# Performance work log

Hardware: AMD Instinct MI355X
Metric: run time of the kernel (lower is better)

Reference implementation:

```python
import jax, jax.numpy as jnp
import numpy as np

EMBED = 256
NHEAD = 8
DFF = 1024
NLAYERS = 1
B, H, W, WS = 4, 128, 128, 16


def _layernorm(x, g, b, eps=1e-5):
    mu = jnp.mean(x, axis=-1, keepdims=True)
    var = jnp.var(x, axis=-1, keepdims=True)
    return (x - mu) * jax.lax.rsqrt(var + eps) * g + b


def _mha(q, k, v, in_w, in_b, out_w, out_b, kpm=None):
    # torch nn.MultiheadAttention (batch_first) with dropout=0
    Bn, L, C = q.shape
    dh = C // NHEAD
    wq, wk, wv = jnp.split(in_w, 3, axis=0)
    bq, bk, bv = jnp.split(in_b, 3, axis=0)
    qh = (q @ wq.T + bq).reshape(Bn, L, NHEAD, dh)
    kh = (k @ wk.T + bk).reshape(Bn, k.shape[1], NHEAD, dh)
    vh = (v @ wv.T + bv).reshape(Bn, v.shape[1], NHEAD, dh)
    scores = jnp.einsum('bqhd,bkhd->bhqk', qh, kh) * (dh ** -0.5)
    if kpm is not None:  # True == masked key
        scores = jnp.where(kpm[:, None, None, :], -jnp.inf, scores)
    attn = jax.nn.softmax(scores, axis=-1)
    out = jnp.einsum('bhqk,bkhd->bqhd', attn, vh).reshape(Bn, L, C)
    return out @ out_w.T + out_b


def _enc_layer(q, k, v, p, kpm=None):
    # post-norm AxisPermutedEncoderLayer, dropout=0
    (in_w, in_b, out_w, out_b, l1w, l1b, l2w, l2b, g1, b1, g2, b2) = p
    src = v + _mha(q, k, v, in_w, in_b, out_w, out_b, kpm)
    src = _layernorm(src, g1, b1)
    ff = jax.nn.relu(src @ l1w.T + l1b) @ l2w.T + l2b
    return _layernorm(src + ff, g2, b2)


def _forward(backbone_memory, defe_feature_filtered, window_size, glob_pos_embed,
             rel_w1, rel_b1, rel_w2, rel_b2,
             in_proj_w, in_proj_b, out_proj_w, out_proj_b,
             lin1_w, lin1_b, lin2_w, lin2_b, ln1_g, ln1_b, ln2_g, ln2_b):
    Bb, C, Hh, Ww = backbone_memory.shape
    ws = window_size
    nwh, nww = Hh // ws, Ww // ws
    nw, T = nwh * nww, ws * ws
    p = (in_proj_w, in_proj_b, out_proj_w, out_proj_b,
         lin1_w, lin1_b, lin2_w, lin2_b, ln1_g, ln1_b, ln2_g, ln2_b)
    # relative position embedding: MLP over normalized in-window (y,x) coords
    ys, xs = jnp.meshgrid(jnp.arange(ws), jnp.arange(ws), indexing='ij')
    coords = jnp.stack([ys, xs], -1).reshape(T, 2).astype(backbone_memory.dtype) / max(ws - 1, 1)
    rel = jax.nn.relu(coords @ rel_w1.T + rel_b1) @ rel_w2.T + rel_b2  # [T,C]
    # window partition -> [B, nw, T, C]
    feats = backbone_memory.reshape(Bb, C, nwh, ws, nww, ws).transpose(0, 2, 4, 1, 3, 5)
    feats = feats.reshape(Bb, nw, C, T).transpose(0, 1, 3, 2)
    gp = glob_pos_embed.reshape(C, nwh, ws, nww, ws).transpose(1, 3, 0, 2, 4)
    gp = gp.reshape(nw, C, T).transpose(0, 2, 1)[None]  # [1,nw,T,C]
    pos = jnp.broadcast_to(gp + rel[None, None], (Bb, nw, T, C))
    # window validity via max-pool of binary map
    pooled = defe_feature_filtered.reshape(Bb, 1, nwh, ws, nww, ws).max(axis=(3, 5))
    valid = pooled.reshape(Bb, nw) > 0  # bool [B,nw]
    x = feats
    for _ in range(NLAYERS):
        # within-window attention over T tokens
        wi = x.reshape(Bb * nw, T, C)
        wp = pos.reshape(Bb * nw, T, C)
        x = _enc_layer(wi + wp, wi + wp, wi, p).reshape(Bb, nw, T, C)
        # cross-window attention over nw windows (per token position)
        ci = x.transpose(0, 2, 1, 3).reshape(Bb * T, nw, C)
        cp = pos.transpose(0, 2, 1, 3).reshape(Bb * T, nw, C)
        kpm = jnp.broadcast_to(~valid[:, None, :], (Bb, T, nw)).reshape(Bb * T, nw)
        x = _enc_layer(ci + cp, ci + cp, ci, p, kpm).reshape(Bb, T, nw, C).transpose(0, 2, 1, 3)
    enc = x.transpose(0, 1, 3, 2).reshape(Bb, nw, C, ws, ws)
    enc = enc * valid.astype(x.dtype)[:, :, None, None, None]
    upd = enc.reshape(Bb, nwh, nww, C, ws, ws).transpose(0, 3, 1, 4, 2, 5).reshape(Bb, C, Hh, Ww)
    return backbone_memory + upd, valid


def setup_inputs() -> dict:
    key = jax.random.key(0)
    ks = jax.random.split(key, 16)
    C, s = EMBED, 0.02
    inp = {}
    inp['backbone_memory'] = jax.random.normal(ks[0], (B, C, H, W), jnp.float32)
    inp['defe_feature_filtered'] = (jax.random.uniform(ks[1], (B, 1, H, W)) < 0.002).astype(jnp.float32)
    inp['window_size'] = WS
    inp['glob_pos_embed'] = jax.random.normal(ks[2], (C, H, W), jnp.float32) * s
    inp['rel_w1'] = jax.random.normal(ks[3], (64, 2), jnp.float32) * s
    inp['rel_b1'] = jnp.zeros((64,), jnp.float32)
    inp['rel_w2'] = jax.random.normal(ks[4], (C, 64), jnp.float32) * s
    inp['rel_b2'] = jnp.zeros((C,), jnp.float32)
    inp['in_proj_w'] = jax.random.normal(ks[5], (3 * C, C), jnp.float32) * s
    inp['in_proj_b'] = jnp.zeros((3 * C,), jnp.float32)
    inp['out_proj_w'] = jax.random.normal(ks[6], (C, C), jnp.float32) * s
    inp['out_proj_b'] = jnp.zeros((C,), jnp.float32)
    inp['lin1_w'] = jax.random.normal(ks[7], (DFF, C), jnp.float32) * s
    inp['lin1_b'] = jnp.zeros((DFF,), jnp.float32)
    inp['lin2_w'] = jax.random.normal(ks[8], (C, DFF), jnp.float32) * s
    inp['lin2_b'] = jnp.zeros((C,), jnp.float32)
    inp['ln1_g'] = jnp.ones((C,), jnp.float32)
    inp['ln1_b'] = jnp.zeros((C,), jnp.float32)
    inp['ln2_g'] = jnp.ones((C,), jnp.float32)
    inp['ln2_b'] = jnp.zeros((C,), jnp.float32)
    return inp


def reference(backbone_memory, defe_feature_filtered, window_size, glob_pos_embed,
              rel_w1, rel_b1, rel_w2, rel_b2,
              in_proj_w, in_proj_b, out_proj_w, out_proj_b,
              lin1_w, lin1_b, lin2_w, lin2_b, ln1_g, ln1_b, ln2_g, ln2_b):
    return _forward(backbone_memory, defe_feature_filtered, window_size, glob_pos_embed,
                    rel_w1, rel_b1, rel_w2, rel_b2,
                    in_proj_w, in_proj_b, out_proj_w, out_proj_b,
                    lin1_w, lin1_b, lin2_w, lin2_b, ln1_g, ln1_b, ln2_g, ln2_b)
```

## Files before the change

### kernel.cpp

```cpp
#include <hip/hip_runtime.h>
#include <hip/hip_bf16.h>

#define CEMB 256
#define NHEAD 8
#define DHEAD 32
#define DFF 1024
#define BB 4
#define HH 128
#define WW 128
#define WSZ 16
#define NWH 8
#define NW 64
#define TT 256
#define NTOK (BB*NW*TT)

typedef __attribute__((ext_vector_type(8))) short bf16x8;
typedef __attribute__((ext_vector_type(4))) float f32x4;

__device__ __forceinline__ float bf2f(unsigned short u){
    union { float f; unsigned int i; } v; v.i = ((unsigned int)u) << 16; return v.f;
}
__device__ __forceinline__ unsigned short f2bf(float f){
    union { float f; unsigned int i; } v; v.f = f;
    unsigned int r = v.i + 0x7fffu + ((v.i >> 16) & 1u);
    return (unsigned short)(r >> 16);
}
__device__ __forceinline__ void unpack8(uint4 v, float* f){
    f[0]=bf2f((unsigned short)(v.x & 0xffff)); f[1]=bf2f((unsigned short)(v.x>>16));
    f[2]=bf2f((unsigned short)(v.y & 0xffff)); f[3]=bf2f((unsigned short)(v.y>>16));
    f[4]=bf2f((unsigned short)(v.z & 0xffff)); f[5]=bf2f((unsigned short)(v.z>>16));
    f[6]=bf2f((unsigned short)(v.w & 0xffff)); f[7]=bf2f((unsigned short)(v.w>>16));
}
__device__ __forceinline__ void async_copy16(const void* g, void* l){
    __builtin_amdgcn_global_load_lds(
        (const __attribute__((address_space(1))) unsigned int*)g,
        (__attribute__((address_space(3))) unsigned int*)l, 16, 0, 0);
}
__device__ __forceinline__ int sgran(int c, int g){ return c*32 + (g ^ (c & 31)); }

__global__ __launch_bounds__(256) void rel_kernel(const float* __restrict__ rw1,
    const float* __restrict__ rb1, const float* __restrict__ rw2,
    const float* __restrict__ rb2, float* __restrict__ rel)
{
    __shared__ float hsh[64];
    int t = blockIdx.x, c = threadIdx.x;
    int ty = t >> 4, tx = t & 15;
    if (c < 64){
        float y = ty*(1.0f/15.0f), xx = tx*(1.0f/15.0f);
        hsh[c] = fmaxf(y*rw1[2*c] + xx*rw1[2*c+1] + rb1[c], 0.0f);
    }
    __syncthreads();
    float acc = rb2[c];
    #pragma unroll 16
    for (int k = 0; k < 64; ++k) acc += hsh[k]*rw2[c*64 + k];
    rel[t*256 + c] = acc;
}

__global__ __launch_bounds__(256) void posT_kernel(const float* __restrict__ gp,
    const float* __restrict__ rel, unsigned short* __restrict__ pos)
{
    __shared__ float tile[8192];
    const int w  = blockIdx.x >> 3;
    const int cq = (blockIdx.x >> 1) & 3, th = blockIdx.x & 1;
    const int c0 = cq << 6, t0 = th << 7, y0 = th << 3;
    const int wh = w >> 3, wwi = w & 7;
    const int tid = threadIdx.x;
    const float* gpb = gp + (size_t)c0*(HH*WW) + (size_t)(wh*16 + y0)*WW + wwi*16;
    #pragma unroll
    for (int i = 0; i < 8; ++i){
        int n = i*256 + tid, slot = n & 31, c = n >> 5;
        int yl = slot >> 2, xg = slot & 3;
        float4 v = *(const float4*)(gpb + (size_t)c*(HH*WW) + yl*WW + xg*4);
        *(float4*)&tile[sgran(c, slot)*4] = v;
    }
    __syncthreads();
    #pragma unroll
    for (int i = 0; i < 4; ++i){
        int n = i*256 + tid, j = n & 7, tl = n >> 3;
        int g = tl >> 2, e = tl & 3;
        const float* rl = rel + (t0 + tl)*256 + c0 + j*8;
        unsigned short o[8];
        #pragma unroll
        for (int m = 0; m < 8; ++m)
            o[m] = f2bf(tile[sgran(j*8 + m, g)*4 + e] + rl[m]);
        *(uint4*)&pos[((size_t)w*256 + t0 + tl)*CEMB + c0 + j*8] = *(uint4*)o;
    }
}

__global__ __launch_bounds__(256) void valid_kernel(const float* __restrict__ defe,
    float* __restrict__ validf, float* __restrict__ tail)
{
    __shared__ float red[4];
    int bw = blockIdx.x; int b = bw >> 6, w = bw & 63;
    int t = threadIdx.x; int ty = t >> 4, tx = t & 15;
    int wh = w >> 3, wwi = w & 7;
    float v = defe[(size_t)b*(HH*WW) + (wh*16+ty)*WW + wwi*16 + tx];
    int lane = t & 63, wave = t >> 6;
    for (int off = 1; off < 64; off <<= 1) v = fmaxf(v, __shfl_xor(v, off));
    if (lane == 0) red[wave] = v;
    __syncthreads();
    if (t == 0){
        float m = fmaxf(fmaxf(red[0], red[1]), fmaxf(red[2], red[3]));
        float r = (m > 0.0f) ? 1.0f : 0.0f;
        validf[bw] = r;
        tail[bw] = r;
    }
}

__global__ __launch_bounds__(256) void partition_kernel(const float* __restrict__ bb,
    unsigned short* __restrict__ x)
{
    __shared__ float tile[8192];
    const int bw = blockIdx.x >> 3;
    const int b = bw >> 6, w = bw & 63;
    const int cq = (blockIdx.x >> 1) & 3, th = blockIdx.x & 1;
    const int c0 = cq << 6, t0 = th << 7, y0 = th << 3;
    const int wh = w >> 3, wwi = w & 7;
    const int tid = threadIdx.x;
    const float* bbb = bb + ((size_t)(b*CEMB + c0))*(HH*WW) + (size_t)(wh*16 + y0)*WW + wwi*16;
    #pragma unroll
    for (int i = 0; i < 8; ++i){
        int n = i*256 + tid, slot = n & 31, c = n >> 5;
        int yl = slot >> 2, xg = slot & 3;
        float4 v = *(const float4*)(bbb + (size_t)c*(HH*WW) + yl*WW + xg*4);
        *(float4*)&tile[sgran(c, slot)*4] = v;
    }
    __syncthreads();
    #pragma unroll
    for (int i = 0; i < 4; ++i){
        int n = i*256 + tid, j = n & 7, tl = n >> 3;
        int g = tl >> 2, e = tl & 3;
        unsigned short o[8];
        #pragma unroll
        for (int m = 0; m < 8; ++m)
            o[m] = f2bf(tile[sgran(j*8 + m, g)*4 + e]);
        *(uint4*)&x[((size_t)bw*256 + t0 + tl)*CEMB + c0 + j*8] = *(uint4*)o;
    }
}

__global__ __launch_bounds__(256) void wcvt_kernel(const float* __restrict__ w,
    unsigned short* __restrict__ o, int n4)
{
    int i = blockIdx.x*256 + threadIdx.x;
    if (i < n4){
        float4 v = ((const float4*)w)[i];
        ushort4 u;
        u.x = f2bf(v.x); u.y = f2bf(v.y); u.z = f2bf(v.z); u.w = f2bf(v.w);
        ((ushort4*)o)[i] = u;
    }
}

__global__ __launch_bounds__(256) void addpos_kernel(const unsigned short* __restrict__ x,
    const unsigned short* __restrict__ pos, unsigned short* __restrict__ xp)
{
    size_t i = ((size_t)blockIdx.x*256 + threadIdx.x) * 8;
    size_t tok = i >> 8; int c = (int)(i & 255);
    size_t pi = ((tok & 16383) << 8) + c;
    uint4 xv = *(const uint4*)&x[i];
    uint4 pv = *(const uint4*)&pos[pi];
    float xf[8], pf[8]; unpack8(xv, xf); unpack8(pv, pf);
    unsigned short o[8];
    #pragma unroll
    for (int j = 0; j < 8; ++j) o[j] = f2bf(xf[j] + pf[j]);
    *(uint4*)&xp[i] = *(uint4*)o;
}

__global__ __launch_bounds__(256) void gemm_mfma(
    const unsigned short* __restrict__ A,
    const unsigned short* __restrict__ A2, int nsplit, int ldA,
    const unsigned short* __restrict__ W, int K,
    const float* __restrict__ bias,
    unsigned short* __restrict__ out, int ldO, int relu)
{
    __shared__ unsigned short As[128*32];
    __shared__ unsigned short Bs[128*32];
    const int m0 = blockIdx.x << 7, n0 = blockIdx.y << 7;
    const int tid = threadIdx.x;
    const int lane = tid & 63, wave = tid >> 6;
    const int wm = wave & 1, wn = wave >> 1;
    const int fl = lane & 15, quad = lane >> 4;

    const unsigned short* Ap = ((n0 < nsplit) ? A : A2) + (size_t)m0*ldA;
    const unsigned short* Wp = W + (size_t)n0*K;

    const int c0 = tid, c1 = tid + 256;
    const int r0 = c0 >> 2, o0 = ((c0 & 3) ^ ((c0 >> 3) & 3)) << 3;
    const int r1 = c1 >> 2, o1 = ((c1 & 3) ^ ((c1 >> 3) & 3)) << 3;
    const int sw = (quad ^ ((fl >> 1) & 3)) << 3;

    f32x4 acc[4][4] = {};

    for (int k0 = 0; k0 < K; k0 += 32){
        async_copy16(Ap + (size_t)r0*ldA + k0 + o0, &As[c0 << 3]);
        async_copy16(Ap + (size_t)r1*ldA + k0 + o1, &As[c1 << 3]);
        async_copy16(Wp + (size_t)r0*K   + k0 + o0, &Bs[c0 << 3]);
        async_copy16(Wp + (size_t)r1*K   + k0 + o1, &Bs[c1 << 3]);
        __syncthreads();
        bf16x8 av[4], bv[4];
        #pragma unroll
        for (int i = 0; i < 4; ++i){
            av[i] = *(const bf16x8*)&As[(wm*64 + i*16 + fl)*32 + sw];
            bv[i] = *(const bf16x8*)&Bs[(wn*64 + i*16 + fl)*32 + sw];
        }
        #pragma unroll
        for (int i = 0; i < 4; ++i)
            #pragma unroll
            for (int j = 0; j < 4; ++j)
                acc[i][j] = __builtin_amdgcn_mfma_f32_16x16x32_bf16(av[i], bv[j], acc[i][j], 0, 0, 0);
        __syncthreads();
    }

    float bj[4];
    #pragma unroll
    for (int j = 0; j < 4; ++j) bj[j] = bias[n0 + wn*64 + j*16 + fl];
    #pragma unroll
    for (int i = 0; i < 4; ++i){
        int mrow = m0 + wm*64 + i*16 + quad*4;
        #pragma unroll
        for (int j = 0; j < 4; ++j){
            int col = n0 + wn*64 + j*16 + fl;
            #pragma unroll
            for (int r = 0; r < 4; ++r){
                float v = acc[i][j][r] + bj[j];
                if (relu) v = fmaxf(v, 0.0f);
                out[(size_t)(mrow + r)*ldO + col] = f2bf(v);
            }
        }
    }
}

__global__ __launch_bounds__(256, 3) void gemm_ln(
    const unsigned short* __restrict__ A, int K,
    const unsigned short* __restrict__ W,
    const float* __restrict__ bias,
    const unsigned short* __restrict__ resid,
    const float* __restrict__ g, const float* __restrict__ b,
    unsigned short* __restrict__ out)
{
    __shared__ unsigned short As[64*32];
    __shared__ unsigned short Bs[256*32];
    __shared__ float psum[4][64];
    __shared__ float psq[4][64];
    const int m0 = blockIdx.x << 6;
    const int tid = threadIdx.x, lane = tid & 63, wave = tid >> 6;
    const int wn = wave;
    const int fl = lane & 15, quad = lane >> 4;

    const unsigned short* Ap = A + (size_t)m0*K;

    const int ra = tid >> 2, oa = ((tid & 3) ^ ((tid >> 3) & 3)) << 3;
    const int sw = (quad ^ ((fl >> 1) & 3)) << 3;

    f32x4 acc[4][4] = {};

    for (int k0 = 0; k0 < K; k0 += 32){
        async_copy16(Ap + (size_t)ra*K + k0 + oa, &As[tid << 3]);
        #pragma unroll
        for (int t = 0; t < 4; ++t){
            int c = tid + t*256;
            int r = c >> 2, o = ((c & 3) ^ ((c >> 3) & 3)) << 3;
            async_copy16(W + (size_t)r*K + k0 + o, &Bs[c << 3]);
        }
        __syncthreads();
        bf16x8 av[4], bv[4];
        #pragma unroll
        for (int i = 0; i < 4; ++i)
            av[i] = *(const bf16x8*)&As[(i*16 + fl)*32 + sw];
        #pragma unroll
        for (int j = 0; j < 4; ++j)
            bv[j] = *(const bf16x8*)&Bs[(wn*64 + j*16 + fl)*32 + sw];
        #pragma unroll
        for (int i = 0; i < 4; ++i)
            #pragma unroll
            for (int j = 0; j < 4; ++j)
                acc[i][j] = __builtin_amdgcn_mfma_f32_16x16x32_bf16(av[i], bv[j], acc[i][j], 0, 0, 0);
        __syncthreads();
    }

    float bcol[4], gcol[4], bbcol[4];
    #pragma unroll
    for (int j = 0; j < 4; ++j){
        int col = wn*64 + j*16 + fl;
        bcol[j] = bias[col]; gcol[j] = g[col]; bbcol[j] = b[col];
    }
    float s[4][4] = {{0}}, sq[4][4] = {{0}};
    #pragma unroll
    for (int i = 0; i < 4; ++i)
        #pragma unroll
        for (int r = 0; r < 4; ++r){
            int row = m0 + i*16 + quad*4 + r;
            #pragma unroll
            for (int j = 0; j < 4; ++j){
                float h = acc[i][j][r] + bcol[j]
                        + bf2f(resid[(size_t)row*256 + wn*64 + j*16 + fl]);
                acc[i][j][r] = h;
                s[i][r] += h; sq[i][r] += h*h;
            }
        }
    #pragma unroll
    for (int i = 0; i < 4; ++i)
        #pragma unroll
        for (int r = 0; r < 4; ++r){
            float ss = s[i][r], qq = sq[i][r];
            ss += __shfl_xor(ss, 1); qq += __shfl_xor(qq, 1);
            ss += __shfl_xor(ss, 2); qq += __shfl_xor(qq, 2);
            ss += __shfl_xor(ss, 4); qq += __shfl_xor(qq, 4);
            ss += __shfl_xor(ss, 8); qq += __shfl_xor(qq, 8);
            if (fl == 0){
                int lr = i*16 + quad*4 + r;
                psum[wn][lr] = ss; psq[wn][lr] = qq;
            }
        }
    __syncthreads();
    #pragma unroll
    for (int i = 0; i < 4; ++i)
        #pragma unroll
        for (int r = 0; r < 4; ++r){
            int lr = i*16 + quad*4 + r;
            float mu  = (psum[0][lr] + psum[1][lr] + psum[2][lr] + psum[3][lr]) * (1.0f/256.0f);
            float var = (psq[0][lr] + psq[1][lr] + psq[2][lr] + psq[3][lr]) * (1.0f/256.0f) - mu*mu;
            float rstd = rsqrtf(var + 1e-5f);
            #pragma unroll
            for (int j = 0; j < 4; ++j){
                int col = wn*64 + j*16 + fl;
                out[(size_t)(m0 + lr)*256 + col] =
                    f2bf((acc[i][j][r] - mu)*rstd*gcol[j] + bbcol[j]);
            }
        }
}

template<int L, bool CROSS>
__global__ __launch_bounds__(256) void attn_mfma(const unsigned short* __restrict__ qkv,
    unsigned short* __restrict__ attn_out, const float* __restrict__ validf)
{
    constexpr int QW  = (L == 256) ? 64 : 16;
    constexpr int MI  = QW / 16;
    constexpr int VTS = L + 8;
    constexpr int LOG = (L == 256) ? 8 : 6;
    __shared__ unsigned short Ks[L*32];
    __shared__ unsigned short Vt[32*VTS];
    __shared__ unsigned short Ps[4*QW*72];

    const int s = blockIdx.x, h = blockIdx.y;
    int base, stride;
    if (CROSS){ base = (s >> 8)*16384 + (s & 255); stride = 256; }
    else      { base = s << 8; stride = 1; }
    const int tid = threadIdx.x, lane = tid & 63, wave = tid >> 6;
    const int fl = lane & 15, quad = lane >> 4;
    const float scale = 0.17677669529663687f;

    for (int cid = tid; cid < L*4; cid += 256){
        int j = cid >> 2, part = cid & 3;
        async_copy16(qkv + (size_t)(base + j*stride)*768 + 256 + h*32 + part*8, &Ks[cid*8]);
    }
    for (int e = tid; e < L*4; e += 256){
        int j = e & (L-1), dp = e >> LOG;
        uint4 vv = *(const uint4*)(qkv + (size_t)(base + j*stride)*768 + 512 + h*32 + dp*8);
        unsigned short tmp[8]; *(uint4*)tmp = vv;
        #pragma unroll
        for (int d = 0; d < 8; ++d) Vt[(dp*8 + d)*VTS + j] = tmp[d];
    }
    __syncthreads();

    bf16x8 qf[MI];
    #pragma unroll
    for (int mi = 0; mi < MI; ++mi){
        int q = wave*QW + mi*16 + fl;
        qf[mi] = *(const bf16x8*)(qkv + (size_t)(base + q*stride)*768 + h*32 + quad*8);
    }
    float vm[4];
    if (CROSS){
        #pragma unroll
        for (int nj = 0; nj < 4; ++nj) vm[nj] = validf[(s >> 8)*64 + nj*16 + fl];
    }

    f32x4 oacc[MI][2] = {};
    float lpart[MI][4] = {};
    unsigned short* Pw = &Ps[wave*QW*72];

    for (int j0 = 0; j0 < L; j0 += 64){
        bf16x8 kf[4];
        #pragma unroll
        for (int nj = 0; nj < 4; ++nj)
            kf[nj] = *(const bf16x8*)&Ks[(j0 + nj*16 + fl)*32 + quad*8];
        f32x4 sacc[MI][4] = {};
        #pragma unroll
        for (int mi = 0; mi < MI; ++mi)
            #pragma unroll
            for (int nj = 0; nj < 4; ++nj)
                sacc[mi][nj] = __builtin_amdgcn_mfma_f32_16x16x32_bf16(qf[mi], kf[nj], sacc[mi][nj], 0, 0, 0);
        #pragma unroll
        for (int mi = 0; mi < MI; ++mi)
            #pragma unroll
            for (int nj = 0; nj < 4; ++nj)
                #pragma unroll
                for (int r = 0; r < 4; ++r){
                    float p = __expf(sacc[mi][nj][r] * scale);
                    if (CROSS) p *= vm[nj];
                    lpart[mi][r] += p;
                    Pw[(mi*16 + quad*4 + r)*72 + nj*16 + fl] = f2bf(p);
                }
        #pragma unroll
        for (int kk = 0; kk < 2; ++kk){
            bf16x8 vf[2];
            #pragma unroll
            for (int nd = 0; nd < 2; ++nd)
                vf[nd] = *(const bf16x8*)&Vt[(nd*16 + fl)*VTS + j0 + kk*32 + quad*8];
            #pragma unroll
            for (int mi = 0; mi < MI; ++mi){
                bf16x8 pf = *(const bf16x8*)&Pw[(mi*16 + fl)*72 + kk*32 + quad*8];
                #pragma unroll
                for (int nd = 0; nd < 2; ++nd)
                    oacc[mi][nd] = __builtin_amdgcn_mfma_f32_16x16x32_bf16(pf, vf[nd], oacc[mi][nd], 0, 0, 0);
            }
        }
    }

    #pragma unroll
    for (int mi = 0; mi < MI; ++mi)
        #pragma unroll
        for (int r = 0; r < 4; ++r){
            float l = lpart[mi][r];
            l += __shfl_xor(l, 1); l += __shfl_xor(l, 2);
            l += __shfl_xor(l, 4); l += __shfl_xor(l, 8);
            lpart[mi][r] = 1.0f / l;
        }
    #pragma unroll
    for (int mi = 0; mi < MI; ++mi)
        #pragma unroll
        for (int nd = 0; nd < 2; ++nd)
            #pragma unroll
            for (int r = 0; r < 4; ++r){
                int q = wave*QW + mi*16 + quad*4 + r;
                attn_out[(size_t)(base + q*stride)*CEMB + h*32 + nd*16 + fl] =
                    f2bf(oacc[mi][nd][r] * lpart[mi][r]);
            }
}

__global__ __launch_bounds__(256) void scatter_kernel(const float* __restrict__ bb,
    const unsigned short* __restrict__ x, const float* __restrict__ validf,
    float* __restrict__ out)
{
    __shared__ float tile[8192];
    const int bw = blockIdx.x >> 3;
    const int b = bw >> 6, w = bw & 63;
    const int cq = (blockIdx.x >> 1) & 3, th = blockIdx.x & 1;
    const int c0 = cq << 6, t0 = th << 7, y0 = th << 3;
    const int wh = w >> 3, wwi = w & 7;
    const int tid = threadIdx.x;
    const float vf = validf[bw];
    #pragma unroll
    for (int i = 0; i < 4; ++i){
        int n = i*256 + tid, j = n & 7, tl = n >> 3;
        int g = tl >> 2, e = tl & 3;
        uint4 xv = *(const uint4*)&x[((size_t)bw*256 + t0 + tl)*CEMB + c0 + j*8];
        float f[8]; unpack8(xv, f);
        #pragma unroll
        for (int m = 0; m < 8; ++m)
            tile[sgran(j*8 + m, g)*4 + e] = f[m];
    }
    __syncthreads();
    const size_t gbase = ((size_t)(b*CEMB + c0))*(HH*WW) + (size_t)(wh*16 + y0)*WW + wwi*16;
    #pragma unroll
    for (int i = 0; i < 8; ++i){
        int n = i*256 + tid, slot = n & 31, c = n >> 5;
        int yl = slot >> 2, xg = slot & 3;
        size_t gi = gbase + (size_t)c*(HH*WW) + yl*WW + xg*4;
        float4 bv = *(const float4*)(bb + gi);
        float4 xv = *(const float4*)&tile[sgran(c, slot)*4];
        float4 ov;
        ov.x = bv.x + vf*xv.x; ov.y = bv.y + vf*xv.y;
        ov.z = bv.z + vf*xv.z; ov.w = bv.w + vf*xv.w;
        *(float4*)(out + gi) = ov;
    }
}

extern "C" void kernel_launch(void* const* d_in, const int* in_sizes, int n_in,
                              void* d_out, int out_size, void* d_ws, size_t ws_size,
                              hipStream_t stream)
{
    (void)in_sizes; (void)n_in; (void)out_size; (void)ws_size;
    const float* backbone = (const float*)d_in[0];
    const float* defe     = (const float*)d_in[1];
    const float* gpe      = (const float*)d_in[3];
    const float* rw1 = (const float*)d_in[4];
    const float* rb1 = (const float*)d_in[5];
    const float* rw2 = (const float*)d_in[6];
    const float* rb2 = (const float*)d_in[7];
    const float* ipw = (const float*)d_in[8];
    const float* ipb = (const float*)d_in[9];
    const float* opw = (const float*)d_in[10];
    const float* opb = (const float*)d_in[11];
    const float* l1w = (const float*)d_in[12];
    const float* l1b = (const float*)d_in[13];
    const float* l2w = (const float*)d_in[14];
    const float* l2b = (const float*)d_in[15];
    const float* g1  = (const float*)d_in[16];
    const float* b1  = (const float*)d_in[17];
    const float* g2  = (const float*)d_in[18];
    const float* b2  = (const float*)d_in[19];

    char* ws = (char*)d_ws;
    unsigned short* pos    = (unsigned short*)(ws);
    unsigned short* x      = (unsigned short*)(ws +   8388608);
    unsigned short* qkv    = (unsigned short*)(ws +  41943040);
    unsigned short* shared_= (unsigned short*)(ws + 142606336);
    float*          validf = (float*)(ws + 176160768);
    unsigned short* ipw16  = (unsigned short*)(ws + 176161792);
    unsigned short* opw16  = (unsigned short*)(ws + 176555008);
    unsigned short* l1w16  = (unsigned short*)(ws + 176686080);
    unsigned short* l2w16  = (unsigned short*)(ws + 177210368);
    float*          rel    = (float*)(ws + 177734656);
    unsigned short* src = qkv;
    unsigned short* ff  = qkv + 16777216;
    float* outf = (float*)d_out;

    wcvt_kernel<<<192, 256, 0, stream>>>(ipw, ipw16, 49152);
    wcvt_kernel<<< 64, 256, 0, stream>>>(opw, opw16, 16384);
    wcvt_kernel<<<256, 256, 0, stream>>>(l1w, l1w16, 65536);
    wcvt_kernel<<<256, 256, 0, stream>>>(l2w, l2w16, 65536);
    rel_kernel<<<256, 256, 0, stream>>>(rw1, rb1, rw2, rb2, rel);
    posT_kernel<<<512, 256, 0, stream>>>(gpe, rel, pos);
    valid_kernel<<<BB*NW, 256, 0, stream>>>(defe, validf, outf + (size_t)BB*CEMB*HH*WW);
    partition_kernel<<<2048, 256, 0, stream>>>(backbone, x);

    for (int layer = 0; layer < 2; ++layer){
        addpos_kernel<<<8192, 256, 0, stream>>>(x, pos, shared_);
        gemm_mfma<<<dim3(512, 6), 256, 0, stream>>>(shared_, x, 512, CEMB, ipw16, CEMB, ipb, qkv, 768, 0);
        if (layer == 0)
            attn_mfma<256, false><<<dim3(BB*NW, NHEAD), 256, 0, stream>>>(qkv, shared_, validf);
        else
            attn_mfma<64, true><<<dim3(BB*TT, NHEAD), 256, 0, stream>>>(qkv, shared_, validf);
        gemm_ln<<<dim3(1024, 1), 256, 0, stream>>>(shared_, CEMB, opw16, opb, x, g1, b1, src);
        for (int ch = 0; ch < 2; ++ch){
            const int BIG = 1 << 30;
            unsigned short* srcC = src + (size_t)ch*8388608;
            gemm_mfma<<<dim3(256, 8), 256, 0, stream>>>(srcC, srcC, BIG, CEMB, l1w16, CEMB, l1b, ff, DFF, 1);
            gemm_ln<<<dim3(512, 1), 256, 0, stream>>>(ff, DFF, l2w16, l2b, srcC, g2, b2,
                                                      x + (size_t)ch*8388608);
        }
    }
    scatter_kernel<<<2048, 256, 0, stream>>>(backbone, x, validf, outf);
}
```

Baseline: 804.2 us.

## Keep attention probabilities in registers via transposed QK^T and lane shuffles

The attention kernel now computes S^T (K as the A operand), packs the exp'd probabilities into bf16 pairs with v_cvt_pk_bf16_f32, and redistributes them across lanes with shuffles to form the PV MFMA operand. This removes the LDS scratch buffer for P and its store/load round trip. It also swizzles the K layout in LDS to avoid bank conflicts, vectorises the validity-mask load, and adds an occupancy hint to launch bounds. The cost is extra shuffle and select instructions per tile and possible register pressure under the new bound.

```diff
diff --git a/kernel.cpp b/kernel.cpp
--- a/kernel.cpp
+++ b/kernel.cpp
@@ -25,6 +25,11 @@
     unsigned int r = v.i + 0x7fffu + ((v.i >> 16) & 1u);
     return (unsigned short)(r >> 16);
 }
+__device__ __forceinline__ unsigned int cvtpk_bf16(float lo, float hi){
+    unsigned int r;
+    asm("v_cvt_pk_bf16_f32 %0, %1, %2" : "=v"(r) : "v"(lo), "v"(hi));
+    return r;
+}
 __device__ __forceinline__ void unpack8(uint4 v, float* f){
     f[0]=bf2f((unsigned short)(v.x & 0xffff)); f[1]=bf2f((unsigned short)(v.x>>16));
     f[2]=bf2f((unsigned short)(v.y & 0xffff)); f[3]=bf2f((unsigned short)(v.y>>16));
@@ -330,7 +335,7 @@
 }
 
 template<int L, bool CROSS>
-__global__ __launch_bounds__(256) void attn_mfma(const unsigned short* __restrict__ qkv,
+__global__ __launch_bounds__(256, 3) void attn_mfma(const unsigned short* __restrict__ qkv,
     unsigned short* __restrict__ attn_out, const float* __restrict__ validf)
 {
     constexpr int QW  = (L == 256) ? 64 : 16;
@@ -339,7 +344,6 @@
     constexpr int LOG = (L == 256) ? 8 : 6;
     __shared__ unsigned short Ks[L*32];
     __shared__ unsigned short Vt[32*VTS];
-    __shared__ unsigned short Ps[4*QW*72];
 
     const int s = blockIdx.x, h = blockIdx.y;
     int base, stride;
@@ -350,7 +354,7 @@
     const float scale = 0.17677669529663687f;
 
     for (int cid = tid; cid < L*4; cid += 256){
-        int j = cid >> 2, part = cid & 3;
+        int j = cid >> 2, part = (cid & 3) ^ ((cid >> 3) & 3);
         async_copy16(qkv + (size_t)(base + j*stride)*768 + 256 + h*32 + part*8, &Ks[cid*8]);
     }
     for (int e = tid; e < L*4; e += 256){
@@ -368,38 +372,47 @@
         int q = wave*QW + mi*16 + fl;
         qf[mi] = *(const bf16x8*)(qkv + (size_t)(base + q*stride)*768 + h*32 + quad*8);
     }
-    float vm[4];
+    float vm[4][4];
     if (CROSS){
         #pragma unroll
-        for (int nj = 0; nj < 4; ++nj) vm[nj] = validf[(s >> 8)*64 + nj*16 + fl];
+        for (int nj = 0; nj < 4; ++nj){
+            float4 v4 = *(const float4*)&validf[(s >> 8)*64 + nj*16 + quad*4];
+            vm[nj][0] = v4.x; vm[nj][1] = v4.y; vm[nj][2] = v4.z; vm[nj][3] = v4.w;
+        }
     }
 
     f32x4 oacc[MI][2] = {};
-    float lpart[MI][4] = {};
-    unsigned short* Pw = &Ps[wave*QW*72];
+    float lpart[MI] = {};
+    const int sw = (quad ^ ((fl >> 1) & 3)) << 3;
+    const int la = fl | ((quad & 1) << 5);
+    const int lb = la + 16;
 
     for (int j0 = 0; j0 < L; j0 += 64){
         bf16x8 kf[4];
         #pragma unroll
         for (int nj = 0; nj < 4; ++nj)
-            kf[nj] = *(const bf16x8*)&Ks[(j0 + nj*16 + fl)*32 + quad*8];
-        f32x4 sacc[MI][4] = {};
-        #pragma unroll
-        for (int mi = 0; mi < MI; ++mi)
+            kf[nj] = *(const bf16x8*)&Ks[(j0 + nj*16 + fl)*32 + sw];
+        unsigned int pk[MI][4][2];
+        #pragma unroll
+        for (int mi = 0; mi < MI; ++mi){
+            f32x4 sacc[4] = {};
             #pragma unroll
             for (int nj = 0; nj < 4; ++nj)
-                sacc[mi][nj] = __builtin_amdgcn_mfma_f32_16x16x32_bf16(qf[mi], kf[nj], sacc[mi][nj], 0, 0, 0);
-        #pragma unroll
-        for (int mi = 0; mi < MI; ++mi)
-            #pragma unroll
-            for (int nj = 0; nj < 4; ++nj)
+                sacc[nj] = __builtin_amdgcn_mfma_f32_16x16x32_bf16(kf[nj], qf[mi], sacc[nj], 0, 0, 0);
+            #pragma unroll
+            for (int nj = 0; nj < 4; ++nj){
+                float p[4];
                 #pragma unroll
                 for (int r = 0; r < 4; ++r){
-                    float p = __expf(sacc[mi][nj][r] * scale);
-                    if (CROSS) p *= vm[nj];
-                    lpart[mi][r] += p;
-                    Pw[(mi*16 + quad*4 + r)*72 + nj*16 + fl] = f2bf(p);
+                    float pv = __expf(sacc[nj][r] * scale);
+                    if (CROSS) pv *= vm[nj][r];
+                    p[r] = pv;
+                    lpart[mi] += pv;
                 }
+                pk[mi][nj][0] = cvtpk_bf16(p[0], p[1]);
+                pk[mi][nj][1] = cvtpk_bf16(p[2], p[3]);
+            }
+        }
         #pragma unroll
         for (int kk = 0; kk < 2; ++kk){
             bf16x8 vf[2];
@@ -408,33 +421,46 @@
                 vf[nd] = *(const bf16x8*)&Vt[(nd*16 + fl)*VTS + j0 + kk*32 + quad*8];
             #pragma unroll
             for (int mi = 0; mi < MI; ++mi){
-                bf16x8 pf = *(const bf16x8*)&Pw[(mi*16 + fl)*72 + kk*32 + quad*8];
+                unsigned int a0 = __shfl(pk[mi][2*kk  ][0], la, 64);
+                unsigned int a1 = __shfl(pk[mi][2*kk  ][1], la, 64);
+                unsigned int a2 = __shfl(pk[mi][2*kk  ][0], lb, 64);
+                unsigned int a3 = __shfl(pk[mi][2*kk  ][1], lb, 64);
+                unsigned int b0 = __shfl(pk[mi][2*kk+1][0], la, 64);
+                unsigned int b1 = __shfl(pk[mi][2*kk+1][1], la, 64);
+                unsigned int b2 = __shfl(pk[mi][2*kk+1][0], lb, 64);
+                unsigned int b3 = __shfl(pk[mi][2*kk+1][1], lb, 64);
+                const bool lo = quad < 2;
+                union { unsigned int u[4]; bf16x8 v; } pu;
+                pu.u[0] = lo ? a0 : b0;
+                pu.u[1] = lo ? a1 : b1;
+                pu.u[2] = lo ? a2 : b2;
+                pu.u[3] = lo ? a3 : b3;
                 #pragma unroll
                 for (int nd = 0; nd < 2; ++nd)
-                    oacc[mi][nd] = __builtin_amdgcn_mfma_f32_16x16x32_bf16(pf, vf[nd], oacc[mi][nd], 0, 0, 0);
-            }
-        }
-    }
-
-    #pragma unroll
-    for (int mi = 0; mi < MI; ++mi)
-        #pragma unroll
-        for (int r = 0; r < 4; ++r){
-            float l = lpart[mi][r];
-            l += __shfl_xor(l, 1); l += __shfl_xor(l, 2);
-            l += __shfl_xor(l, 4); l += __shfl_xor(l, 8);
-            lpart[mi][r] = 1.0f / l;
-        }
-    #pragma unroll
-    for (int mi = 0; mi < MI; ++mi)
+                    oacc[mi][nd] = __builtin_amdgcn_mfma_f32_16x16x32_bf16(pu.v, vf[nd], oacc[mi][nd], 0, 0, 0);
+            }
+        }
+    }
+
+    #pragma unroll
+    for (int mi = 0; mi < MI; ++mi){
+        float l = lpart[mi];
+        l += __shfl_xor(l, 16);
+        l += __shfl_xor(l, 32);
+        l = 1.0f / l;
+        float li[4];
+        #pragma unroll
+        for (int r = 0; r < 4; ++r)
+            li[r] = __shfl(l, quad*4 + r, 64);
         #pragma unroll
         for (int nd = 0; nd < 2; ++nd)
             #pragma unroll
             for (int r = 0; r < 4; ++r){
                 int q = wave*QW + mi*16 + quad*4 + r;
                 attn_out[(size_t)(base + q*stride)*CEMB + h*32 + nd*16 + fl] =
-                    f2bf(oacc[mi][nd][r] * lpart[mi][r]);
-            }
+                    f2bf(oacc[mi][nd][r] * li[r]);
+            }
+    }
 }
 
 __global__ __launch_bounds__(256) void scatter_kernel(const float* __restrict__ bb,
```

Result: no change. 792.4 us (-1.5%).
